# Performance work log

Hardware: AMD Instinct MI355X
Metric: run time of the kernel (lower is better)

Reference implementation:

```python
import jax, jax.numpy as jnp
import numpy as np
from jax import lax

# Model dims (match init_kwargs)
B, CH, H, W = 32, 2, 32, 16
C_LEN, P_LEN, T_LEN = 3, 4, 4
POI_N, PT_F, T_FEAT, RP_N = 12, 9, 28, 4
OUTC = 8  # ResPlus out_channels
EPS = 1e-5


def conv1x1(x, w, b):
    # x: [B,C,H,W], w: [O,C,1,1] -> [B,O,H,W]
    return jnp.einsum('bchw,oc->bohw', x, w[:, :, 0, 0]) + b[None, :, None, None]


def conv3x3(x, w, b):
    y = lax.conv_general_dilated(x, w, (1, 1), 'SAME',
                                 dimension_numbers=('NCHW', 'OIHW', 'NCHW'))
    return y + b[None, :, None, None]


def bn(x, g, b, m, v):
    # eval-mode BatchNorm2d with running stats
    s = g / jnp.sqrt(v + EPS)
    return x * s[None, :, None, None] + (b - m * s)[None, :, None, None]


def forward(x, convc_w, convc_b, convp_w, convp_b, convt_w, convt_b,
            tm_w, tm_b, tf_w, tf_b, poi_w, poi_b,
            bn1_g, bn1_b, bn1_m, bn1_v, conv1_w, conv1_b,
            rp_bn1_g, rp_bn1_b, rp_bn1_m, rp_bn1_v, rp_conv1_w, rp_conv1_b,
            rp_bn2_g, rp_bn2_b, rp_bn2_m, rp_bn2_v, rp_conv2_w, rp_conv2_b,
            plus_w, plus_b, bn2_g, bn2_b, bn2_m, bn2_v, conv2_w, conv2_b):
    cut1 = CH * C_LEN
    cut2 = cut1 + CH * P_LEN
    cut3 = cut2 + CH * T_LEN
    c = conv1x1(x[:, :cut1], convc_w, convc_b)
    p = conv1x1(x[:, cut1:cut2], convp_w, convp_b)
    t = conv1x1(x[:, cut2:cut3], convt_w, convt_b)
    poi_in = x[:, -(POI_N + 31):-31]
    time_in = x[:, -31:]
    # PoI_trans / Time_trans
    tx = jax.nn.relu(conv1x1(time_in, tm_w, tm_b))
    tx = jax.nn.relu(conv1x1(tx, tf_w, tf_b))          # [B,1,H,W]
    poi_time = conv1x1(tx * poi_in, poi_w, poi_b)      # broadcast tile over PoI_N
    cpt = jnp.concatenate([c, p, t, poi_time], axis=1)
    cpt = bn(jax.nn.relu(cpt), bn1_g, bn1_b, bn1_m, bn1_v)
    cpt = conv1x1(cpt, conv1_w, conv1_b)               # [B,64,H,W]
    # ResPlus applied RP_N times with SHARED weights (self.net in a loop)
    plus_wf = plus_w.reshape(OUTC * H * W, -1)         # [8*H*W, 64*H*W]
    for _ in range(RP_N):
        z1 = conv3x3(jax.nn.relu(bn(cpt, rp_bn1_g, rp_bn1_b, rp_bn1_m, rp_bn1_v)),
                     rp_conv1_w, rp_conv1_b)           # [B,56,H,W]
        z2 = bn(jax.nn.relu(cpt), rp_bn1_g, rp_bn1_b, rp_bn1_m, rp_bn1_v)
        # plus_conv: full-map (H,W) kernel -> 1x1 spatial, i.e. a big GEMM
        z2 = (z2.reshape(B, -1) @ plus_wf.T + plus_b).reshape(B, OUTC, H, W)
        z3 = jax.nn.relu(bn(jnp.concatenate([z1, z2], axis=1),
                            rp_bn2_g, rp_bn2_b, rp_bn2_m, rp_bn2_v))
        cpt = conv3x3(z3, rp_conv2_w, rp_conv2_b) + cpt
    cpt2 = bn(jax.nn.relu(cpt), bn2_g, bn2_b, bn2_m, bn2_v)
    return jnp.tanh(conv1x1(cpt2, conv2_w, conv2_b))   # [B,2,H,W]


def setup_inputs() -> dict:
    key = jax.random.key(0)
    ks = iter(jax.random.split(key, 48))
    def rn(shape, s=0.05):
        return jax.random.normal(next(ks), shape, jnp.float32) * s
    def bnp(n):
        return (1.0 + rn((n,), 0.02), rn((n,)), rn((n,)),
                1.0 + 0.1 * jax.random.uniform(next(ks), (n,), jnp.float32))
    total_c = CH * (C_LEN + P_LEN + T_LEN) + POI_N + 31
    inp = {'x': jax.random.normal(next(ks), (B, total_c, H, W), jnp.float32)}
    inp['convc_w'], inp['convc_b'] = rn((64, CH * C_LEN, 1, 1)), rn((64,))
    inp['convp_w'], inp['convp_b'] = rn((64, CH * P_LEN, 1, 1)), rn((64,))
    inp['convt_w'], inp['convt_b'] = rn((64, CH * T_LEN, 1, 1)), rn((64,))
    inp['tm_w'], inp['tm_b'] = rn((T_FEAT, 31, 1, 1)), rn((T_FEAT,))
    inp['tf_w'], inp['tf_b'] = rn((1, T_FEAT, 1, 1)), rn((1,))
    inp['poi_w'], inp['poi_b'] = rn((PT_F, POI_N, 1, 1)), rn((PT_F,))
    inp['bn1_g'], inp['bn1_b'], inp['bn1_m'], inp['bn1_v'] = bnp(192 + PT_F)
    inp['conv1_w'], inp['conv1_b'] = rn((64, 192 + PT_F, 1, 1)), rn((64,))
    inp['rp_bn1_g'], inp['rp_bn1_b'], inp['rp_bn1_m'], inp['rp_bn1_v'] = bnp(64)
    inp['rp_conv1_w'], inp['rp_conv1_b'] = rn((64 - OUTC, 64, 3, 3)), rn((64 - OUTC,))
    inp['rp_bn2_g'], inp['rp_bn2_b'], inp['rp_bn2_m'], inp['rp_bn2_v'] = bnp(64)
    inp['rp_conv2_w'], inp['rp_conv2_b'] = rn((64, 64, 3, 3)), rn((64,))
    inp['plus_w'], inp['plus_b'] = rn((OUTC * H * W, 64, H, W), 0.01), rn((OUTC * H * W,))
    inp['bn2_g'], inp['bn2_b'], inp['bn2_m'], inp['bn2_v'] = bnp(64)
    inp['conv2_w'], inp['conv2_b'] = rn((2, 64, 1, 1)), rn((2,))
    return inp


def reference(x, convc_w, convc_b, convp_w, convp_b, convt_w, convt_b,
              tm_w, tm_b, tf_w, tf_b, poi_w, poi_b,
              bn1_g, bn1_b, bn1_m, bn1_v, conv1_w, conv1_b,
              rp_bn1_g, rp_bn1_b, rp_bn1_m, rp_bn1_v, rp_conv1_w, rp_conv1_b,
              rp_bn2_g, rp_bn2_b, rp_bn2_m, rp_bn2_v, rp_conv2_w, rp_conv2_b,
              plus_w, plus_b, bn2_g, bn2_b, bn2_m, bn2_v, conv2_w, conv2_b):
    return forward(x, convc_w, convc_b, convp_w, convp_b, convt_w, convt_b,
                   tm_w, tm_b, tf_w, tf_b, poi_w, poi_b,
                   bn1_g, bn1_b, bn1_m, bn1_v, conv1_w, conv1_b,
                   rp_bn1_g, rp_bn1_b, rp_bn1_m, rp_bn1_v, rp_conv1_w, rp_conv1_b,
                   rp_bn2_g, rp_bn2_b, rp_bn2_m, rp_bn2_v, rp_conv2_w, rp_conv2_b,
                   plus_w, plus_b, bn2_g, bn2_b, bn2_m, bn2_v, conv2_w, conv2_b)
```

## Files before the change

kernel.cpp:

```cpp
#include <hip/hip_runtime.h>
#include <cmath>
#include <cstdint>

typedef __bf16 bf16x8 __attribute__((ext_vector_type(8)));
typedef float  f32x4  __attribute__((ext_vector_type(4)));
typedef float  f32x16 __attribute__((ext_vector_type(16)));

#define EPSF 1e-5f

__global__ __launch_bounds__(64) void head_kernel(
    const float* __restrict__ x,
    const float* __restrict__ cw, const float* __restrict__ cb,
    const float* __restrict__ pw, const float* __restrict__ pb,
    const float* __restrict__ tw, const float* __restrict__ tb,
    const float* __restrict__ tmw, const float* __restrict__ tmb,
    const float* __restrict__ tfw, const float* __restrict__ tfb,
    const float* __restrict__ poiw, const float* __restrict__ poib,
    const float* __restrict__ g1, const float* __restrict__ bb1,
    const float* __restrict__ m1, const float* __restrict__ v1,
    const float* __restrict__ w1, const float* __restrict__ b1c,
    float* __restrict__ cpt)
{
    int pix = blockIdx.x;
    int b = pix >> 9, p = pix & 511;
    int t = threadIdx.x;

    __shared__ float xs[65];
    __shared__ float tx1[28];
    __shared__ float y[201];
    __shared__ float tx2s;

    for (int c = t; c < 65; c += 64)
        xs[c] = x[(b * 65 + c) * 512 + p];
    __syncthreads();

    if (t < 28) {
        float acc = tmb[t];
        for (int j = 0; j < 31; ++j) acc += tmw[t * 31 + j] * xs[34 + j];
        tx1[t] = fmaxf(acc, 0.f);
    }
    __syncthreads();
    if (t == 0) {
        float acc = tfb[0];
        for (int j = 0; j < 28; ++j) acc += tfw[j] * tx1[j];
        tx2s = fmaxf(acc, 0.f);
    }
    __syncthreads();
    float tx2 = tx2s;

    {
        float acc = cb[t];
        for (int j = 0; j < 6; ++j) acc += cw[t * 6 + j] * xs[j];
        y[t] = acc;
    }
    {
        float acc = pb[t];
        for (int j = 0; j < 8; ++j) acc += pw[t * 8 + j] * xs[6 + j];
        y[64 + t] = acc;
    }
    {
        float acc = tb[t];
        for (int j = 0; j < 8; ++j) acc += tw[t * 8 + j] * xs[14 + j];
        y[128 + t] = acc;
    }
    if (t < 9) {
        float acc = poib[t];
        for (int j = 0; j < 12; ++j) acc += poiw[t * 12 + j] * (tx2 * xs[22 + j]);
        y[192 + t] = acc;
    }
    for (int c = t; c < 201; c += 64) {
        float s  = g1[c] * rsqrtf(v1[c] + EPSF);
        float tt = bb1[c] - m1[c] * s;
        y[c] = fmaxf(y[c], 0.f) * s + tt;
    }
    __syncthreads();

    float acc = b1c[t];
    const float* wrow = w1 + t * 201;
    for (int c = 0; c < 201; ++c) acc += wrow[c] * y[c];
    cpt[(b * 64 + t) * 512 + p] = acc;
}

__global__ __launch_bounds__(256) void wconv_tiled_kernel(const float* __restrict__ w,
                                                          __bf16* __restrict__ wt)
{
    __shared__ __bf16 lds[32 * 528];
    int nt = blockIdx.x;
    int kg = blockIdx.y;
    int t  = threadIdx.x;

    int klo  = t * 2;
    int g16l = klo >> 4;
    int hi   = (klo >> 3) & 1;
    int e    = klo & 7;
    __bf16* d = &lds[g16l * 528 + hi * 256 + e];
    const float* src0 = w + (long)(nt * 32) * 32768 + kg * 512 + klo;
    for (int r = 0; r < 32; ++r) {
        float2 v = *(const float2*)(src0 + (long)r * 32768);
        d[r * 8 + 0] = (__bf16)v.x;
        d[r * 8 + 1] = (__bf16)v.y;
    }
    __syncthreads();

#pragma unroll
    for (int j = 0; j < 8; ++j) {
        int fid = j * 256 + t;
        int gl = fid >> 6;
        int l  = fid & 63;
        int k16 = kg * 32 + gl;
        int it  = k16 & 127;
        int ks  = k16 >> 7;
        bf16x8 v = *(const bf16x8*)&lds[gl * 528 + (l >> 5) * 256 + (l & 31) * 8];
        long off = ((long)(it * 16 + ks) * 128 + nt) * 512 + l * 8;
        *(bf16x8*)(wt + off) = v;
    }
}

__global__ void prep_tiled_kernel(const float* __restrict__ cpt,
                                  const float* __restrict__ g, const float* __restrict__ bb,
                                  const float* __restrict__ m, const float* __restrict__ v,
                                  const float* __restrict__ plus_b,
                                  __bf16* __restrict__ a_t, float* __restrict__ z2)
{
    int i = blockIdx.x * blockDim.x + threadIdx.x;
    if (i < 32 * 64 * 512) {
        int b = i >> 15, c = (i >> 9) & 63, p = i & 511;
        float s  = g[c] * rsqrtf(v[c] + EPSF);
        float tt = bb[c] - m[c] * s;
        float val = fmaxf(cpt[i], 0.f) * s + tt;
        int k = c * 512 + p;
        int idx = ((k >> 4) * 64 + ((k >> 3) & 1) * 32 + b) * 8 + (k & 7);
        a_t[idx] = (__bf16)val;
    }
    if (i < 32 * 4096) {
        z2[i] = plus_b[i & 4095];
    }
}

__global__ void prep_kernel(const float* __restrict__ cpt,
                            const float* __restrict__ g, const float* __restrict__ bb,
                            const float* __restrict__ m, const float* __restrict__ v,
                            const float* __restrict__ plus_b,
                            __bf16* __restrict__ a_bf, float* __restrict__ z2)
{
    int i = blockIdx.x * blockDim.x + threadIdx.x;
    if (i < 32 * 64 * 512) {
        int c = (i >> 9) & 63;
        float s  = g[c] * rsqrtf(v[c] + EPSF);
        float tt = bb[c] - m[c] * s;
        a_bf[i] = (__bf16)(fmaxf(cpt[i], 0.f) * s + tt);
    }
    if (i < 32 * 4096) {
        z2[i] = plus_b[i & 4095];
    }
}

__global__ __launch_bounds__(256) void gemm_kernel(const __bf16* __restrict__ a_bf,
                                                   const float* __restrict__ plus_w,
                                                   float* __restrict__ z2)
{
    int wave = threadIdx.x >> 6;
    int lane = threadIdx.x & 63;
    int gw = blockIdx.x * 4 + wave;
    int nt = gw & 127;
    int ks = gw >> 7;
    int r32 = lane & 31;
    int hi  = lane >> 5;
    int n = nt * 32 + r32;
    long k0 = (long)ks * 2048 + hi * 8;

    const float*  wp = plus_w + (long)n * 32768 + k0;
    const bf16x8* ap = (const bf16x8*)(a_bf + (long)r32 * 32768 + k0);

    f32x16 acc = {};
#pragma unroll 4
    for (int it = 0; it < 128; ++it) {
        f32x4 w0 = *(const f32x4*)(wp + it * 16);
        f32x4 w1 = *(const f32x4*)(wp + it * 16 + 4);
        bf16x8 bfr;
#pragma unroll
        for (int j = 0; j < 4; ++j) { bfr[j] = (__bf16)w0[j]; bfr[j + 4] = (__bf16)w1[j]; }
        bf16x8 afr = ap[it * 2];
        acc = __builtin_amdgcn_mfma_f32_32x32x16_bf16(afr, bfr, acc, 0, 0, 0);
    }
#pragma unroll
    for (int r = 0; r < 16; ++r) {
        int brow = (r & 3) + 8 * (r >> 2) + 4 * hi;
        atomicAdd(&z2[brow * 4096 + n], acc[r]);
    }
}

__global__ __launch_bounds__(256) void gemm_reg_kernel(const __bf16* __restrict__ a_t,
                                                       const __bf16* __restrict__ w_t,
                                                       float* __restrict__ z2)
{
    int wave = threadIdx.x >> 6;
    int lane = threadIdx.x & 63;
    int gw = blockIdx.x * 4 + wave;
    int nt = gw & 127;
    int ks = gw >> 7;
    int r32 = lane & 31;
    int hi  = lane >> 5;
    int n = nt * 32 + r32;

    const bf16x8* ap = (const bf16x8*)(a_t + (long)(ks * 128) * 512 + lane * 8);
    const bf16x8* wp = (const bf16x8*)(w_t + ((long)ks * 128 + nt) * 512 + lane * 8);

    f32x16 acc = {};
#pragma unroll 8
    for (int it = 0; it < 128; ++it) {
        bf16x8 afr = ap[(long)it * 64];
        bf16x8 bfr = wp[(long)it * 131072];
        acc = __builtin_amdgcn_mfma_f32_32x32x16_bf16(afr, bfr, acc, 0, 0, 0);
    }

#pragma unroll
    for (int r = 0; r < 16; ++r) {
        int brow = (r & 3) + 8 * (r >> 2) + 4 * hi;
        atomicAdd(&z2[brow * 4096 + n], acc[r]);
    }
}

__global__ __launch_bounds__(512) void conv1_kernel(const float* __restrict__ cpt,
                                                    const float* __restrict__ g, const float* __restrict__ bb,
                                                    const float* __restrict__ m, const float* __restrict__ v,
                                                    const float* __restrict__ w,
                                                    const float* __restrict__ bias,
                                                    float* __restrict__ z1)
{
    int b  = blockIdx.x;
    int og = blockIdx.y;
    int p  = threadIdx.x;
    int h = p >> 4, wc = p & 15;
    int o0 = og * 4;

    __shared__ float ss[64], ts[64];
    if (p < 64) {
        float s = g[p] * rsqrtf(v[p] + EPSF);
        ss[p] = s;
        ts[p] = bb[p] - m[p] * s;
    }
    __syncthreads();

    float a0 = bias[o0], a1 = bias[o0 + 1], a2 = bias[o0 + 2], a3 = bias[o0 + 3];
    const float* rb = cpt + b * 64 * 512;
    for (int c = 0; c < 64; ++c) {
        const float* rc = rb + c * 512;
        float s = ss[c], tt = ts[c];
        float rv[9];
#pragma unroll
        for (int dh = -1; dh <= 1; ++dh)
#pragma unroll
            for (int dw = -1; dw <= 1; ++dw) {
                int hh = h + dh, ww = wc + dw;
                bool ok = (hh >= 0) & (hh < 32) & (ww >= 0) & (ww < 16);
                rv[(dh + 1) * 3 + (dw + 1)] = ok ? fmaxf(rc[hh * 16 + ww] * s + tt, 0.f) : 0.f;
            }
#pragma unroll
        for (int tp = 0; tp < 9; ++tp) {
            a0 += rv[tp] * w[((o0    ) * 64 + c) * 9 + tp];
            a1 += rv[tp] * w[((o0 + 1) * 64 + c) * 9 + tp];
            a2 += rv[tp] * w[((o0 + 2) * 64 + c) * 9 + tp];
            a3 += rv[tp] * w[((o0 + 3) * 64 + c) * 9 + tp];
        }
    }
    float* zb = z1 + ((b * 56 + o0) * 512) + p;
    zb[0] = a0; zb[512] = a1; zb[1024] = a2; zb[1536] = a3;
}

__global__ void prep2_kernel(const float* __restrict__ z1, const float* __restrict__ z2,
                             const float* __restrict__ g, const float* __restrict__ bb,
                             const float* __restrict__ m, const float* __restrict__ v,
                             __bf16* __restrict__ z3)
{
    int i = blockIdx.x * blockDim.x + threadIdx.x;
    if (i >= 32 * 64 * 512) return;
    int b = i >> 15, c = (i >> 9) & 63, p = i & 511;
    float val = (c < 56) ? z1[(b * 56 + c) * 512 + p]
                         : z2[b * 4096 + (c - 56) * 512 + p];
    float s  = g[c] * rsqrtf(v[c] + EPSF);
    float tt = bb[c] - m[c] * s;
    z3[i] = (__bf16)fmaxf(val * s + tt, 0.f);
}

__global__ __launch_bounds__(512) void conv2_kernel(const __bf16* __restrict__ z3,
                                                    const float* __restrict__ w,
                                                    const float* __restrict__ bias,
                                                    float* __restrict__ cpt)
{
    int b  = blockIdx.x;
    int og = blockIdx.y;
    int p  = threadIdx.x;
    int h = p >> 4, wc = p & 15;
    int o0 = og * 4;
    float a0 = bias[o0], a1 = bias[o0 + 1], a2 = bias[o0 + 2], a3 = bias[o0 + 3];
    const __bf16* rb = z3 + b * 64 * 512;
    for (int c = 0; c < 64; ++c) {
        const __bf16* rc = rb + c * 512;
        float rv[9];
#pragma unroll
        for (int dh = -1; dh <= 1; ++dh)
#pragma unroll
            for (int dw = -1; dw <= 1; ++dw) {
                int hh = h + dh, ww = wc + dw;
                bool ok = (hh >= 0) & (hh < 32) & (ww >= 0) & (ww < 16);
                rv[(dh + 1) * 3 + (dw + 1)] = ok ? (float)rc[hh * 16 + ww] : 0.f;
            }
#pragma unroll
        for (int tp = 0; tp < 9; ++tp) {
            a0 += rv[tp] * w[((o0    ) * 64 + c) * 9 + tp];
            a1 += rv[tp] * w[((o0 + 1) * 64 + c) * 9 + tp];
            a2 += rv[tp] * w[((o0 + 2) * 64 + c) * 9 + tp];
            a3 += rv[tp] * w[((o0 + 3) * 64 + c) * 9 + tp];
        }
    }
    float* cb_ = cpt + ((b * 64 + o0) * 512) + p;
    cb_[0]    += a0;
    cb_[512]  += a1;
    cb_[1024] += a2;
    cb_[1536] += a3;
}

__global__ void tail_kernel(const float* __restrict__ cpt,
                            const float* __restrict__ g, const float* __restrict__ bb,
                            const float* __restrict__ m, const float* __restrict__ v,
                            const float* __restrict__ w2, const float* __restrict__ b2,
                            float* __restrict__ out)
{
    int i = blockIdx.x * blockDim.x + threadIdx.x;
    if (i >= 32 * 512) return;
    int b = i >> 9, p = i & 511;
    float a0 = b2[0], a1 = b2[1];
    for (int c = 0; c < 64; ++c) {
        float s  = g[c] * rsqrtf(v[c] + EPSF);
        float tt = bb[c] - m[c] * s;
        float y = fmaxf(cpt[(b * 64 + c) * 512 + p], 0.f) * s + tt;
        a0 += w2[c] * y;
        a1 += w2[64 + c] * y;
    }
    out[(b * 2 + 0) * 512 + p] = tanhf(a0);
    out[(b * 2 + 1) * 512 + p] = tanhf(a1);
}

extern "C" void kernel_launch(void* const* d_in, const int* in_sizes, int n_in,
                              void* d_out, int out_size, void* d_ws, size_t ws_size,
                              hipStream_t stream)
{
#define IN(i) ((const float*)d_in[i])
    float*  cpt  = (float*)d_ws;
    __bf16* a_t  = (__bf16*)((char*)d_ws + (size_t)4 * 1024 * 1024);
    __bf16* z3   = a_t;
    float*  z1   = (float*)((char*)d_ws + (size_t)6 * 1024 * 1024);
    float*  z2   = z1 + 32 * 56 * 512;
    __bf16* w_t  = (__bf16*)((char*)d_ws + (size_t)10 * 1024 * 1024);

    const bool cacheW = ws_size >= (size_t)266 * 1024 * 1024;

    if (cacheW)
        wconv_tiled_kernel<<<dim3(128, 64), 256, 0, stream>>>(IN(31), w_t);

    head_kernel<<<16384, 64, 0, stream>>>(
        IN(0), IN(1), IN(2), IN(3), IN(4), IN(5), IN(6), IN(7), IN(8), IN(9), IN(10),
        IN(11), IN(12), IN(13), IN(14), IN(15), IN(16), IN(17), IN(18), cpt);

    for (int it = 0; it < 4; ++it) {
        if (cacheW) {
            prep_tiled_kernel<<<4096, 256, 0, stream>>>(cpt, IN(19), IN(20), IN(21), IN(22),
                                                        IN(32), a_t, z2);
            gemm_reg_kernel<<<512, 256, 0, stream>>>(a_t, w_t, z2);
        } else {
            prep_kernel<<<4096, 256, 0, stream>>>(cpt, IN(19), IN(20), IN(21), IN(22),
                                                  IN(32), a_t, z2);
            gemm_kernel<<<512, 256, 0, stream>>>(a_t, IN(31), z2);
        }
        conv1_kernel<<<dim3(32, 14), 512, 0, stream>>>(cpt, IN(19), IN(20), IN(21), IN(22),
                                                       IN(23), IN(24), z1);
        prep2_kernel<<<4096, 256, 0, stream>>>(z1, z2, IN(25), IN(26), IN(27), IN(28), z3);
        conv2_kernel<<<dim3(32, 16), 512, 0, stream>>>(z3, IN(29), IN(30), cpt);
    }

    tail_kernel<<<64, 256, 0, stream>>>(cpt, IN(33), IN(34), IN(35), IN(36),
                                        IN(37), IN(38), (float*)d_out);
#undef IN
}
```

Measured before the change: 1.723 ms.

## Double GEMM split-K and replace atomics with partial buffers reduced in prep2

Split the K dimension of the plus_conv GEMM into 32 chunks instead of 16, doubling the grid to 1024 blocks, and write each chunk's partial result to its own slice of a new buffer instead of using atomicAdd. The bias add and the reduction over the 32 partials move into prep2_kernel, so the z2 initialization is dropped from the prep kernels. The aim is more waves in flight to stream the large weight matrix and no atomic contention. The cost is extra partial-buffer traffic, 32 reads per output element in prep2, and a larger workspace threshold for the cached-weight path.

```diff
diff --git a/kernel.cpp b/kernel.cpp
--- a/kernel.cpp
+++ b/kernel.cpp
@@ -7,6 +7,9 @@
 typedef float  f32x16 __attribute__((ext_vector_type(16)));
 
 #define EPSF 1e-5f
+
+#define NSPLIT 32
+#define KSTEPS 64
 
 __global__ __launch_bounds__(64) void head_kernel(
     const float* __restrict__ x,
@@ -108,10 +111,10 @@
         int gl = fid >> 6;
         int l  = fid & 63;
         int k16 = kg * 32 + gl;
-        int it  = k16 & 127;
-        int ks  = k16 >> 7;
+        int it  = k16 & (KSTEPS - 1);
+        int ks  = k16 >> 6;
         bf16x8 v = *(const bf16x8*)&lds[gl * 528 + (l >> 5) * 256 + (l & 31) * 8];
-        long off = ((long)(it * 16 + ks) * 128 + nt) * 512 + l * 8;
+        long off = ((long)(it * NSPLIT + ks) * 128 + nt) * 512 + l * 8;
         *(bf16x8*)(wt + off) = v;
     }
 }
@@ -119,45 +122,35 @@
 __global__ void prep_tiled_kernel(const float* __restrict__ cpt,
                                   const float* __restrict__ g, const float* __restrict__ bb,
                                   const float* __restrict__ m, const float* __restrict__ v,
-                                  const float* __restrict__ plus_b,
-                                  __bf16* __restrict__ a_t, float* __restrict__ z2)
+                                  __bf16* __restrict__ a_t)
 {
     int i = blockIdx.x * blockDim.x + threadIdx.x;
-    if (i < 32 * 64 * 512) {
-        int b = i >> 15, c = (i >> 9) & 63, p = i & 511;
-        float s  = g[c] * rsqrtf(v[c] + EPSF);
-        float tt = bb[c] - m[c] * s;
-        float val = fmaxf(cpt[i], 0.f) * s + tt;
-        int k = c * 512 + p;
-        int idx = ((k >> 4) * 64 + ((k >> 3) & 1) * 32 + b) * 8 + (k & 7);
-        a_t[idx] = (__bf16)val;
-    }
-    if (i < 32 * 4096) {
-        z2[i] = plus_b[i & 4095];
-    }
+    if (i >= 32 * 64 * 512) return;
+    int b = i >> 15, c = (i >> 9) & 63, p = i & 511;
+    float s  = g[c] * rsqrtf(v[c] + EPSF);
+    float tt = bb[c] - m[c] * s;
+    float val = fmaxf(cpt[i], 0.f) * s + tt;
+    int k = c * 512 + p;
+    int idx = ((k >> 4) * 64 + ((k >> 3) & 1) * 32 + b) * 8 + (k & 7);
+    a_t[idx] = (__bf16)val;
 }
 
 __global__ void prep_kernel(const float* __restrict__ cpt,
                             const float* __restrict__ g, const float* __restrict__ bb,
                             const float* __restrict__ m, const float* __restrict__ v,
-                            const float* __restrict__ plus_b,
-                            __bf16* __restrict__ a_bf, float* __restrict__ z2)
+                            __bf16* __restrict__ a_bf)
 {
     int i = blockIdx.x * blockDim.x + threadIdx.x;
-    if (i < 32 * 64 * 512) {
-        int c = (i >> 9) & 63;
-        float s  = g[c] * rsqrtf(v[c] + EPSF);
-        float tt = bb[c] - m[c] * s;
-        a_bf[i] = (__bf16)(fmaxf(cpt[i], 0.f) * s + tt);
-    }
-    if (i < 32 * 4096) {
-        z2[i] = plus_b[i & 4095];
-    }
+    if (i >= 32 * 64 * 512) return;
+    int c = (i >> 9) & 63;
+    float s  = g[c] * rsqrtf(v[c] + EPSF);
+    float tt = bb[c] - m[c] * s;
+    a_bf[i] = (__bf16)(fmaxf(cpt[i], 0.f) * s + tt);
 }
 
 __global__ __launch_bounds__(256) void gemm_kernel(const __bf16* __restrict__ a_bf,
                                                    const float* __restrict__ plus_w,
-                                                   float* __restrict__ z2)
+                                                   float* __restrict__ z2p)
 {
     int wave = threadIdx.x >> 6;
     int lane = threadIdx.x & 63;
@@ -167,14 +160,14 @@
     int r32 = lane & 31;
     int hi  = lane >> 5;
     int n = nt * 32 + r32;
-    long k0 = (long)ks * 2048 + hi * 8;
+    long k0 = (long)ks * 1024 + hi * 8;
 
     const float*  wp = plus_w + (long)n * 32768 + k0;
     const bf16x8* ap = (const bf16x8*)(a_bf + (long)r32 * 32768 + k0);
 
     f32x16 acc = {};
 #pragma unroll 4
-    for (int it = 0; it < 128; ++it) {
+    for (int it = 0; it < KSTEPS; ++it) {
         f32x4 w0 = *(const f32x4*)(wp + it * 16);
         f32x4 w1 = *(const f32x4*)(wp + it * 16 + 4);
         bf16x8 bfr;
@@ -186,13 +179,13 @@
 #pragma unroll
     for (int r = 0; r < 16; ++r) {
         int brow = (r & 3) + 8 * (r >> 2) + 4 * hi;
-        atomicAdd(&z2[brow * 4096 + n], acc[r]);
-    }
-}
-
-__global__ __launch_bounds__(256) void gemm_reg_kernel(const __bf16* __restrict__ a_t,
-                                                       const __bf16* __restrict__ w_t,
-                                                       float* __restrict__ z2)
+        z2p[((ks * 32 + brow) * 4096) + n] = acc[r];
+    }
+}
+
+__global__ __launch_bounds__(256, 4) void gemm_reg_kernel(const __bf16* __restrict__ a_t,
+                                                          const __bf16* __restrict__ w_t,
+                                                          float* __restrict__ z2p)
 {
     int wave = threadIdx.x >> 6;
     int lane = threadIdx.x & 63;
@@ -203,21 +196,21 @@
     int hi  = lane >> 5;
     int n = nt * 32 + r32;
 
-    const bf16x8* ap = (const bf16x8*)(a_t + (long)(ks * 128) * 512 + lane * 8);
-    const bf16x8* wp = (const bf16x8*)(w_t + ((long)ks * 128 + nt) * 512 + lane * 8);
+    const bf16x8* ap = (const bf16x8*)a_t + (long)ks * KSTEPS * 64 + lane;
+    const bf16x8* wp = (const bf16x8*)w_t + ((long)ks * 128 + nt) * 64 + lane;
 
     f32x16 acc = {};
-#pragma unroll 8
-    for (int it = 0; it < 128; ++it) {
+#pragma unroll 4
+    for (int it = 0; it < KSTEPS; ++it) {
         bf16x8 afr = ap[(long)it * 64];
-        bf16x8 bfr = wp[(long)it * 131072];
+        bf16x8 bfr = wp[(long)it * 262144];
         acc = __builtin_amdgcn_mfma_f32_32x32x16_bf16(afr, bfr, acc, 0, 0, 0);
     }
 
 #pragma unroll
     for (int r = 0; r < 16; ++r) {
         int brow = (r & 3) + 8 * (r >> 2) + 4 * hi;
-        atomicAdd(&z2[brow * 4096 + n], acc[r]);
+        z2p[((ks * 32 + brow) * 4096) + n] = acc[r];
     }
 }
 
@@ -268,7 +261,8 @@
     zb[0] = a0; zb[512] = a1; zb[1024] = a2; zb[1536] = a3;
 }
 
-__global__ void prep2_kernel(const float* __restrict__ z1, const float* __restrict__ z2,
+__global__ void prep2_kernel(const float* __restrict__ z1, const float* __restrict__ z2p,
+                             const float* __restrict__ plus_b,
                              const float* __restrict__ g, const float* __restrict__ bb,
                              const float* __restrict__ m, const float* __restrict__ v,
                              __bf16* __restrict__ z3)
@@ -276,8 +270,17 @@
     int i = blockIdx.x * blockDim.x + threadIdx.x;
     if (i >= 32 * 64 * 512) return;
     int b = i >> 15, c = (i >> 9) & 63, p = i & 511;
-    float val = (c < 56) ? z1[(b * 56 + c) * 512 + p]
-                         : z2[b * 4096 + (c - 56) * 512 + p];
+    float val;
+    if (c < 56) {
+        val = z1[(b * 56 + c) * 512 + p];
+    } else {
+        int n = (c - 56) * 512 + p;
+        val = plus_b[n];
+        const float* zp = z2p + b * 4096 + n;
+#pragma unroll
+        for (int ks = 0; ks < NSPLIT; ++ks)
+            val += zp[(long)ks * 32 * 4096];
+    }
     float s  = g[c] * rsqrtf(v[c] + EPSF);
     float tt = bb[c] - m[c] * s;
     z3[i] = (__bf16)fmaxf(val * s + tt, 0.f);
@@ -351,10 +354,10 @@
     __bf16* a_t  = (__bf16*)((char*)d_ws + (size_t)4 * 1024 * 1024);
     __bf16* z3   = a_t;
     float*  z1   = (float*)((char*)d_ws + (size_t)6 * 1024 * 1024);
-    float*  z2   = z1 + 32 * 56 * 512;
-    __bf16* w_t  = (__bf16*)((char*)d_ws + (size_t)10 * 1024 * 1024);
-
-    const bool cacheW = ws_size >= (size_t)266 * 1024 * 1024;
+    float*  z2p  = (float*)((char*)d_ws + (size_t)10 * 1024 * 1024);
+    __bf16* w_t  = (__bf16*)((char*)d_ws + (size_t)32 * 1024 * 1024);
+
+    const bool cacheW = ws_size >= (size_t)288 * 1024 * 1024;
 
     if (cacheW)
         wconv_tiled_kernel<<<dim3(128, 64), 256, 0, stream>>>(IN(31), w_t);
@@ -365,17 +368,15 @@
 
     for (int it = 0; it < 4; ++it) {
         if (cacheW) {
-            prep_tiled_kernel<<<4096, 256, 0, stream>>>(cpt, IN(19), IN(20), IN(21), IN(22),
-                                                        IN(32), a_t, z2);
-            gemm_reg_kernel<<<512, 256, 0, stream>>>(a_t, w_t, z2);
+            prep_tiled_kernel<<<4096, 256, 0, stream>>>(cpt, IN(19), IN(20), IN(21), IN(22), a_t);
+            gemm_reg_kernel<<<1024, 256, 0, stream>>>(a_t, w_t, z2p);
         } else {
-            prep_kernel<<<4096, 256, 0, stream>>>(cpt, IN(19), IN(20), IN(21), IN(22),
-                                                  IN(32), a_t, z2);
-            gemm_kernel<<<512, 256, 0, stream>>>(a_t, IN(31), z2);
+            prep_kernel<<<4096, 256, 0, stream>>>(cpt, IN(19), IN(20), IN(21), IN(22), a_t);
+            gemm_kernel<<<1024, 256, 0, stream>>>(a_t, IN(31), z2p);
         }
         conv1_kernel<<<dim3(32, 14), 512, 0, stream>>>(cpt, IN(19), IN(20), IN(21), IN(22),
                                                        IN(23), IN(24), z1);
-        prep2_kernel<<<4096, 256, 0, stream>>>(z1, z2, IN(25), IN(26), IN(27), IN(28), z3);
+        prep2_kernel<<<4096, 256, 0, stream>>>(z1, z2p, IN(32), IN(25), IN(26), IN(27), IN(28), z3);
         conv2_kernel<<<dim3(32, 16), 512, 0, stream>>>(z3, IN(29), IN(30), cpt);
     }
 
```

Result: no change. 1.752 ms (+1.7%).
